# Performance work log

Hardware: AMD Instinct MI355X
Metric: run time of the kernel (lower is better)

## Reference

```python
import jax, jax.numpy as jnp
import numpy as np

B, S, T = 4096, 512, 32


def setup_inputs() -> dict:
    key = jax.random.key(0)
    k1, k2, k3, k4, k5 = jax.random.split(key, 5)
    emissions = jax.random.normal(k1, (B, S, T), dtype=jnp.float32)
    tags = jax.random.randint(k2, (B, S), 0, T)
    mask = jnp.ones((B, S), dtype=bool)
    transitions = jax.random.normal(k3, (T, T), dtype=jnp.float32)
    start_transitions = jax.random.normal(k4, (T,), dtype=jnp.float32)
    end_transitions = jax.random.normal(k5, (T,), dtype=jnp.float32)
    return {
        "emissions": emissions,
        "tags": tags,
        "mask": mask,
        "transitions": transitions,
        "start_transitions": start_transitions,
        "end_transitions": end_transitions,
    }


def _score_sentence(emissions, tags, mask, transitions, start_transitions, end_transitions):
    # gold path score, fully vectorized over batch and time
    t0 = tags[:, 0]
    score = start_transitions[t0]
    score = score + jnp.take_along_axis(emissions[:, 0], t0[:, None], axis=1)[:, 0]
    maskf = mask[:, 1:].astype(emissions.dtype)  # [B, S-1]
    trans_sc = transitions[tags[:, :-1], tags[:, 1:]]  # [B, S-1]
    emit_sc = jnp.take_along_axis(emissions[:, 1:], tags[:, 1:, None], axis=2)[..., 0]
    score = score + ((trans_sc + emit_sc) * maskf).sum(axis=1)
    last_idx = mask.sum(axis=1).astype(jnp.int32) - 1  # [B]
    last_tags = jnp.take_along_axis(tags, last_idx[:, None], axis=1)[:, 0]
    score = score + end_transitions[last_tags]
    return score  # [B]


def _forward_algorithm(emissions, mask, transitions, start_transitions, end_transitions):
    # log partition via lax.scan over time; state is [B, T]
    score0 = start_transitions + emissions[:, 0]  # [B, T]
    em_rest = jnp.swapaxes(emissions[:, 1:], 0, 1)  # [S-1, B, T]
    mk_rest = jnp.swapaxes(mask[:, 1:], 0, 1)  # [S-1, B]

    def step(score, xs):
        em_i, m_i = xs
        # score[b,prev] + transitions[prev,next] + em_i[b,next]
        next_score = jax.nn.logsumexp(
            score[:, :, None] + transitions[None, :, :] + em_i[:, None, :], axis=1
        )
        score = jnp.where(m_i[:, None], next_score, score)
        return score, None

    score, _ = jax.lax.scan(step, score0, (em_rest, mk_rest))
    return jax.nn.logsumexp(score + end_transitions, axis=1)  # [B]


def reference(emissions, tags, mask, transitions, start_transitions, end_transitions):
    gold = _score_sentence(emissions, tags, mask, transitions, start_transitions, end_transitions)
    fwd = _forward_algorithm(emissions, mask, transitions, start_transitions, end_transitions)
    return (fwd - gold).mean()
```

## Files before the change

### kernel.cpp

```cpp
#include <hip/hip_runtime.h>
#include <hip/hip_bf16.h>


#define L2E 1.4426950408889634f
#define LN2 0.6931471805599453f

__global__ void crf_zero(float* out) { out[0] = 0.0f; }

__global__ __launch_bounds__(256) void crf_kernel(
    const float* __restrict__ emissions,
    const int*   __restrict__ tags,
    const float* __restrict__ transitions,
    const float* __restrict__ start_t,
    const float* __restrict__ end_t,
    float* __restrict__ out)
{
    constexpr int S = 512, T = 32;

    __shared__ float trans_raw[T * T];
    __shared__ float u_lds[8][T];
    __shared__ float res_lds[8];

    const int tid   = threadIdx.x;
    const int lane  = tid & 63;
    const int t     = lane & 31;
    const int slot  = tid >> 5;
    const int hbase = lane & 32;
    const long b    = (long)blockIdx.x * 8 + slot;

    #pragma unroll
    for (int k = 0; k < 4; ++k)
        trans_raw[tid + 256 * k] = transitions[tid + 256 * k];
    __syncthreads();

    float vv[T];
    #pragma unroll
    for (int k = 0; k < T; ++k)
        vv[k] = __builtin_amdgcn_exp2f(transitions[k * T + t] * L2E);

    const float* em_base = emissions + b * (long)(S * T) + t;
    const int*   tg_base = tags + b * S;

    float em0     = em_base[0];
    float em_cur  = em_base[T];
    int   tag_prev = tg_base[0];
    int   tag_cur  = tg_base[1];

    float startv = start_t[t];
    float r    = (startv + em0) * L2E;
    float offs = 0.0f;
    float gold = __shfl(startv, hbase + tag_prev, 64)
               + __shfl(em0,    hbase + tag_prev, 64);

    for (int i = 1; i < S; ++i) {
        int ip = (i + 1 < S) ? (i + 1) : (S - 1);
        float em_next  = em_base[(long)ip * T];
        int   tag_next = tg_base[ip];

        float u = __builtin_amdgcn_exp2f(r);
        u_lds[slot][t] = u;
        __builtin_amdgcn_wave_barrier();
        const float4* up = reinterpret_cast<const float4*>(&u_lds[slot][0]);
        float s0 = 0.f, s1 = 0.f, s2 = 0.f, s3 = 0.f;
        #pragma unroll
        for (int j = 0; j < 8; ++j) {
            float4 uv = up[j];
            s0 = fmaf(uv.x, vv[4 * j + 0], s0);
            s1 = fmaf(uv.y, vv[4 * j + 1], s1);
            s2 = fmaf(uv.z, vv[4 * j + 2], s2);
            s3 = fmaf(uv.w, vv[4 * j + 3], s3);
        }
        __builtin_amdgcn_wave_barrier();
        float s = (s0 + s1) + (s2 + s3);

        float r_raw = fmaf(em_cur, L2E, __builtin_amdgcn_logf(s));
        float bk = __shfl(r_raw, hbase, 64);
        r = r_raw - bk;
        offs += bk;

        gold += trans_raw[tag_prev * 32 + tag_cur]
              + __shfl(em_cur, hbase + tag_cur, 64);

        tag_prev = tag_cur;
        tag_cur  = tag_next;
        em_cur   = em_next;
    }

    float endv = end_t[t];
    gold += __shfl(endv, hbase + tag_prev, 64);

    float x = r + endv * L2E;
    float m = x;
    #pragma unroll
    for (int d = 16; d >= 1; d >>= 1) m = fmaxf(m, __shfl_xor(m, d, 64));
    float e = __builtin_amdgcn_exp2f(x - m);
    #pragma unroll
    for (int d = 16; d >= 1; d >>= 1) e += __shfl_xor(e, d, 64);
    float fwd2 = offs + m + __builtin_amdgcn_logf(e);

    float resv = fwd2 * LN2 - gold;

    if (t == 0) res_lds[slot] = resv;
    __syncthreads();
    if (tid == 0) {
        float acc = 0.0f;
        #pragma unroll
        for (int k = 0; k < 8; ++k) acc += res_lds[k];
        atomicAdd(out, acc * (1.0f / 4096.0f));
    }
}

extern "C" void kernel_launch(void* const* d_in, const int* in_sizes, int n_in,
                              void* d_out, int out_size, void* d_ws, size_t ws_size,
                              hipStream_t stream) {
    const float* emissions   = (const float*)d_in[0];
    const int*   tags        = (const int*)d_in[1];
    const float* transitions = (const float*)d_in[3];
    const float* start_t     = (const float*)d_in[4];
    const float* end_t       = (const float*)d_in[5];
    float* out = (float*)d_out;

    crf_zero<<<1, 1, 0, stream>>>(out);
    crf_kernel<<<512, 256, 0, stream>>>(emissions, tags, transitions,
                                        start_t, end_t, out);
}
```

Measured before the change: 477.6 us.

## Prefetch emissions and tags 8 steps ahead and delay log-sum normalization

Replaces the one-step-ahead load of emissions and tags with an 8-deep register ring buffer, unrolled by 8, so global-load latency is hidden across several recurrence steps. The per-step normalizer shuffle is moved off the critical path by subtracting the previous step's offset, and the dot-product accumulation is split into 8 partial sums for more ILP. The zero-init kernel is replaced with hipMemsetAsync. This raises register pressure, and the delayed offset lets values drift slightly before renormalization.

```diff
diff --git a/kernel.cpp b/kernel.cpp
--- a/kernel.cpp
+++ b/kernel.cpp
@@ -4,8 +4,7 @@
 
 #define L2E 1.4426950408889634f
 #define LN2 0.6931471805599453f
-
-__global__ void crf_zero(float* out) { out[0] = 0.0f; }
+#define PD  8
 
 __global__ __launch_bounds__(256) void crf_kernel(
     const float* __restrict__ emissions,
@@ -41,50 +40,69 @@
     const float* em_base = emissions + b * (long)(S * T) + t;
     const int*   tg_base = tags + b * S;
 
-    float em0     = em_base[0];
-    float em_cur  = em_base[T];
+    float em0      = em_base[0];
     int   tag_prev = tg_base[0];
-    int   tag_cur  = tg_base[1];
 
-    float startv = start_t[t];
-    float r    = (startv + em0) * L2E;
-    float offs = 0.0f;
+    float em_buf[PD];
+    int   tag_buf[PD];
+    #pragma unroll
+    for (int j = 0; j < PD; ++j) {
+        em_buf[j]  = em_base[(long)(1 + j) * T];
+        tag_buf[j] = tg_base[1 + j];
+    }
+
+    float startv  = start_t[t];
+    float r       = (startv + em0) * L2E;
+    float offs    = 0.0f;
+    float bk_prev = 0.0f;
     float gold = __shfl(startv, hbase + tag_prev, 64)
                + __shfl(em0,    hbase + tag_prev, 64);
 
-    for (int i = 1; i < S; ++i) {
-        int ip = (i + 1 < S) ? (i + 1) : (S - 1);
-        float em_next  = em_base[(long)ip * T];
-        int   tag_next = tg_base[ip];
+    auto step = [&](int i, int bi) {
+        float em_cur  = em_buf[bi];
+        int   tag_cur = tag_buf[bi];
+        int ip = i + PD; ip = (ip < S) ? ip : (S - 1);
+        em_buf[bi]  = em_base[(long)ip * T];
+        tag_buf[bi] = tg_base[ip];
 
         float u = __builtin_amdgcn_exp2f(r);
         u_lds[slot][t] = u;
         __builtin_amdgcn_wave_barrier();
         const float4* up = reinterpret_cast<const float4*>(&u_lds[slot][0]);
         float s0 = 0.f, s1 = 0.f, s2 = 0.f, s3 = 0.f;
+        float s4 = 0.f, s5 = 0.f, s6 = 0.f, s7 = 0.f;
         #pragma unroll
-        for (int j = 0; j < 8; ++j) {
-            float4 uv = up[j];
-            s0 = fmaf(uv.x, vv[4 * j + 0], s0);
-            s1 = fmaf(uv.y, vv[4 * j + 1], s1);
-            s2 = fmaf(uv.z, vv[4 * j + 2], s2);
-            s3 = fmaf(uv.w, vv[4 * j + 3], s3);
+        for (int j = 0; j < 4; ++j) {
+            float4 ua = up[2 * j];
+            float4 ub = up[2 * j + 1];
+            s0 = fmaf(ua.x, vv[8 * j + 0], s0);
+            s1 = fmaf(ua.y, vv[8 * j + 1], s1);
+            s2 = fmaf(ua.z, vv[8 * j + 2], s2);
+            s3 = fmaf(ua.w, vv[8 * j + 3], s3);
+            s4 = fmaf(ub.x, vv[8 * j + 4], s4);
+            s5 = fmaf(ub.y, vv[8 * j + 5], s5);
+            s6 = fmaf(ub.z, vv[8 * j + 6], s6);
+            s7 = fmaf(ub.w, vv[8 * j + 7], s7);
         }
         __builtin_amdgcn_wave_barrier();
-        float s = (s0 + s1) + (s2 + s3);
+        float s = ((s0 + s1) + (s2 + s3)) + ((s4 + s5) + (s6 + s7));
 
         float r_raw = fmaf(em_cur, L2E, __builtin_amdgcn_logf(s));
-        float bk = __shfl(r_raw, hbase, 64);
-        r = r_raw - bk;
-        offs += bk;
+        r     = r_raw - bk_prev;
+        offs += bk_prev;
+        bk_prev = __shfl(r, hbase, 64);
 
         gold += trans_raw[tag_prev * 32 + tag_cur]
               + __shfl(em_cur, hbase + tag_cur, 64);
+        tag_prev = tag_cur;
+    };
 
-        tag_prev = tag_cur;
-        tag_cur  = tag_next;
-        em_cur   = em_next;
+    for (int ii = 1; ii < 505; ii += 8) {
+        #pragma unroll
+        for (int j = 0; j < 8; ++j) step(ii + j, j);
     }
+    #pragma unroll
+    for (int j = 0; j < 7; ++j) step(505 + j, j);
 
     float endv = end_t[t];
     gold += __shfl(endv, hbase + tag_prev, 64);
@@ -120,7 +138,7 @@
     const float* end_t       = (const float*)d_in[5];
     float* out = (float*)d_out;
 
-    crf_zero<<<1, 1, 0, stream>>>(out);
+    hipMemsetAsync(out, 0, sizeof(float), stream);
     crf_kernel<<<512, 256, 0, stream>>>(emissions, tags, transitions,
                                         start_t, end_t, out);
 }
```

Result: faster. 449.9 us (-5.8%).
